# Optimization experiments

Hardware: AMD Instinct MI355X
Metric: run time of the kernel (lower is better)

## Reference

```python
import jax, jax.numpy as jnp
import numpy as np
from jax import lax

B, T_CAP, V, WD, H, L, IC = 256, 51, 10000, 512, 512, 2, 2048


def setup_inputs() -> dict:
    key = jax.random.key(0)
    ks = jax.random.split(key, 16)
    u01 = lambda k, s: jax.random.uniform(k, s, jnp.float32, -0.1, 0.1)
    sc = 1.0 / np.sqrt(H)
    uh = lambda k, s: jax.random.uniform(k, s, jnp.float32, -sc, sc)
    image_code = jax.random.normal(ks[0], (B, IC), jnp.float32)
    captions = jax.random.randint(ks[1], (B, T_CAP), 0, V)
    cap_lens = jax.random.randint(ks[2], (B,), 2, T_CAP + 1)
    cap_lens = cap_lens.at[0].set(T_CAP)  # guarantees max len == T_CAP (static scan length)
    return {
        "image_code": image_code,
        "captions": captions,
        "cap_lens": cap_lens,
        "embed_w": u01(ks[3], (V, WD)),
        "init_w": uh(ks[4], (L * H, IC)),
        "init_b": uh(ks[5], (L * H,)),
        "w_ih0": uh(ks[6], (3 * H, WD + IC)),
        "w_hh0": uh(ks[7], (3 * H, H)),
        "b_ih0": uh(ks[8], (3 * H,)),
        "b_hh0": uh(ks[9], (3 * H,)),
        "w_ih1": uh(ks[10], (3 * H, H)),
        "w_hh1": uh(ks[11], (3 * H, H)),
        "b_ih1": uh(ks[12], (3 * H,)),
        "b_hh1": uh(ks[13], (3 * H,)),
        "fc_w": u01(ks[14], (V, H)),
        "fc_b": jnp.zeros((V,), jnp.float32),
    }


def _gru_cell(x, h, w_ih, w_hh, b_ih, b_hh):
    # torch nn.GRU cell: gates ordered (r, z, n)
    gi = x @ w_ih.T + b_ih
    gh = h @ w_hh.T + b_hh
    i_r, i_z, i_n = jnp.split(gi, 3, axis=-1)
    h_r, h_z, h_n = jnp.split(gh, 3, axis=-1)
    r = jax.nn.sigmoid(i_r + h_r)
    z = jax.nn.sigmoid(i_z + h_z)
    n = jnp.tanh(i_n + r * h_n)
    return (1.0 - z) * n + z * h


def reference(image_code, captions, cap_lens, embed_w, init_w, init_b,
              w_ih0, w_hh0, b_ih0, b_hh0, w_ih1, w_hh1, b_ih1, b_hh1,
              fc_w, fc_b):
    b = image_code.shape[0]
    # sort by caption length, descending (ragged batch shrink in original)
    order = jnp.argsort(-cap_lens)
    sorted_lens = cap_lens[order]
    caps = captions[order]
    img = image_code[order]
    # init hidden: (L, B, H)
    h0 = (img @ init_w.T + init_b).reshape(b, L, H).transpose(1, 0, 2)
    lengths = sorted_lens - 1                      # decode steps per example
    T = captions.shape[1] - 1                      # static; equals lengths[0] by construction
    emb = embed_w[caps]                            # (B, T+1, WD)
    xs = jnp.swapaxes(emb[:, :T, :], 0, 1)         # (T, B, WD)
    mask_ts = jnp.arange(T)[:, None] < lengths[None, :]  # (T, B)
    params = [(w_ih0, w_hh0, b_ih0, b_hh0), (w_ih1, w_hh1, b_ih1, b_hh1)]

    def step(h, inp):
        x_emb, m = inp
        layer_in = jnp.concatenate([img, x_emb], axis=-1)  # (B, IC+WD)
        new_h = []
        for l, (wi, wh, bi, bh) in enumerate(params):
            hl = _gru_cell(layer_in, h[l], wi, wh, bi, bh)
            new_h.append(hl)
            layer_in = hl
        h_new = jnp.stack(new_h)
        # rows past their length keep their old hidden (equivalent to the
        # torch loop never touching rows beyond real_batch_size)
        h_new = jnp.where(m[None, :, None], h_new, h)
        preds = layer_in @ fc_w.T + fc_b           # dropout is identity in eval
        preds = jnp.where(m[:, None], preds, 0.0)  # predictions stay zero past length
        return h_new, preds

    _, preds = lax.scan(step, h0, (xs, mask_ts))   # preds: (T, B, V)
    predictions = jnp.swapaxes(preds, 0, 1)        # (B, T, V)
    return predictions, caps, lengths, order
```

## Files before the change

kernel.cpp:

```cpp
#include <hip/hip_runtime.h>
#include <hip/hip_bf16.h>

#define BB   256
#define TCAP 51
#define TT   50
#define VV   10000
#define WDIM 512
#define HH   512
#define ICC  2048
#define G3H  1536
#define FCP  8

typedef __attribute__((ext_vector_type(8))) short short8v;
typedef __attribute__((ext_vector_type(4))) float f32x4;

__device__ __forceinline__ unsigned short f2bf(float f) {
    unsigned u; __builtin_memcpy(&u, &f, 4);
    unsigned r = (u + 0x7FFFu + ((u >> 16) & 1u)) >> 16;
    return (unsigned short)r;
}
__device__ __forceinline__ float bf2f(unsigned short b) {
    unsigned u = ((unsigned)b) << 16; float f; __builtin_memcpy(&f, &u, 4); return f;
}
__device__ __forceinline__ short8v cvt8(float4 a, float4 b) {
    union { unsigned short u[8]; short8v v; } o;
    o.u[0] = f2bf(a.x); o.u[1] = f2bf(a.y); o.u[2] = f2bf(a.z); o.u[3] = f2bf(a.w);
    o.u[4] = f2bf(b.x); o.u[5] = f2bf(b.y); o.u[6] = f2bf(b.z); o.u[7] = f2bf(b.w);
    return o.v;
}
__device__ __forceinline__ float sigm(float x) { return 1.f / (1.f + expf(-x)); }

__global__ void sort_kernel(const int* __restrict__ cap_lens, const int* __restrict__ captions,
                            int* __restrict__ order_ws, int* __restrict__ len_ws,
                            int* __restrict__ caps_ws, float* __restrict__ out,
                            size_t predN) {
    __shared__ int s_order[BB];
    int i = threadIdx.x;
    int li = cap_lens[i];
    int rank = 0;
    for (int j = 0; j < BB; ++j) {
        int lj = cap_lens[j];
        rank += (lj > li) || (lj == li && j < i);
    }
    s_order[rank] = i;
    __syncthreads();
    int src = s_order[i];
    order_ws[i] = src;
    int len = cap_lens[src] - 1;
    len_ws[i] = len;
    for (int t = 0; t < TCAP; ++t) {
        int c = captions[src * TCAP + t];
        caps_ws[i * TCAP + t] = c;
        out[predN + (size_t)i * TCAP + t] = (float)c;
    }
    out[predN + (size_t)BB * TCAP + i]      = (float)len;
    out[predN + (size_t)BB * TCAP + BB + i] = (float)src;
}

__global__ void gather_imgb(const float* __restrict__ image_code, const int* __restrict__ order_ws,
                            unsigned short* __restrict__ imgb) {
    int i = blockIdx.x * 256 + threadIdx.x;
    int p = i >> 8, c8 = (i & 255) << 3;
    const float* s = image_code + (size_t)order_ws[p] * ICC + c8;
    float4 v0 = *(const float4*)s, v1 = *(const float4*)(s + 4);
    *(short8v*)&imgb[(size_t)p * ICC + c8] = cvt8(v0, v1);
}

__global__ void cvt_mat(const float* __restrict__ src, int src_ld, int src_off,
                        unsigned short* __restrict__ dst, int dst_ld, int dst_off,
                        int cols, int n8) {
    int i = blockIdx.x * 256 + threadIdx.x;
    if (i < n8) {
        int cpr = cols >> 3;
        int row = i / cpr, c8 = (i - row * cpr) << 3;
        const float* s = src + (size_t)row * src_ld + src_off + c8;
        float4 v0 = *(const float4*)s, v1 = *(const float4*)(s + 4);
        *(short8v*)&dst[(size_t)row * dst_ld + dst_off + c8] = cvt8(v0, v1);
    }
}

__global__ __launch_bounds__(256) void gemm_front(
    const unsigned short* __restrict__ imgb,
    const unsigned short* __restrict__ wcomb,
    const float* __restrict__ init_b,
    const float* __restrict__ b_ih0,
    unsigned short* __restrict__ h0s0,
    unsigned short* __restrict__ h1s0,
    float* __restrict__ gi_img) {
    const int p0 = blockIdx.y * 64;
    const int c0 = blockIdx.x * 64;
    const int tid = threadIdx.x;
    __shared__ unsigned short As[64][64 + FCP], Bs[64][64 + FCP];
    const int lane = tid & 63, w = tid >> 6;
    f32x4 acc[4] = {};
    for (int k0 = 0; k0 < ICC; k0 += 64) {
#pragma unroll
        for (int v = 0; v < 2; ++v) {
            int e = tid + v * 256;
            int rr = e >> 3, kk = (e & 7) * 8;
            *(short8v*)&As[rr][kk] = *(const short8v*)&imgb[(size_t)(p0 + rr) * ICC + k0 + kk];
            *(short8v*)&Bs[rr][kk] = *(const short8v*)&wcomb[(size_t)(c0 + rr) * ICC + k0 + kk];
        }
        __syncthreads();
#pragma unroll
        for (int ks = 0; ks < 64; ks += 32) {
            short8v a = *(const short8v*)&As[w * 16 + (lane & 15)][ks + (lane >> 4) * 8];
#pragma unroll
            for (int n = 0; n < 4; ++n) {
                short8v b = *(const short8v*)&Bs[n * 16 + (lane & 15)][ks + (lane >> 4) * 8];
                acc[n] = __builtin_amdgcn_mfma_f32_16x16x32_bf16(a, b, acc[n], 0, 0, 0);
            }
        }
        __syncthreads();
    }
#pragma unroll
    for (int n = 0; n < 4; ++n) {
        int cc = c0 + n * 16 + (lane & 15);
#pragma unroll
        for (int r = 0; r < 4; ++r) {
            int pr = p0 + w * 16 + (lane >> 4) * 4 + r;
            float v = acc[n][r];
            if (cc < 1024) {
                v += init_b[cc];
                unsigned short b = f2bf(v);
                if (cc < 512) h0s0[(size_t)pr * 512 + cc] = b;
                else          h1s0[(size_t)pr * 512 + (cc - 512)] = b;
            } else {
                gi_img[(size_t)pr * G3H + (cc - 1024)] = v + b_ih0[cc - 1024];
            }
        }
    }
}

__global__ __launch_bounds__(256) void gemm_giemb(
    const unsigned short* __restrict__ embb,
    const unsigned short* __restrict__ wihe,
    const float* __restrict__ gi_img,
    const int* __restrict__ caps_ws, const int* __restrict__ len_ws,
    float* __restrict__ gi_all) {
    const int r0 = blockIdx.y * 64;
    const int t = r0 >> 8, p0 = r0 & 255;
    if (len_ws[p0] <= t) return;
    const int c0 = blockIdx.x * 64;
    const int tid = threadIdx.x;
    __shared__ unsigned short As[64][64 + FCP], Bs[64][64 + FCP];
    __shared__ int s_arow[64];
    if (tid < 64) s_arow[tid] = caps_ws[(p0 + tid) * TCAP + t];
    __syncthreads();
    const int lane = tid & 63, w = tid >> 6;
    f32x4 acc[4] = {};
    for (int k0 = 0; k0 < WDIM; k0 += 64) {
#pragma unroll
        for (int v = 0; v < 2; ++v) {
            int e = tid + v * 256;
            int rr = e >> 3, kk = (e & 7) * 8;
            *(short8v*)&As[rr][kk] = *(const short8v*)&embb[(size_t)s_arow[rr] * WDIM + k0 + kk];
            *(short8v*)&Bs[rr][kk] = *(const short8v*)&wihe[(size_t)(c0 + rr) * WDIM + k0 + kk];
        }
        __syncthreads();
#pragma unroll
        for (int ks = 0; ks < 64; ks += 32) {
            short8v a = *(const short8v*)&As[w * 16 + (lane & 15)][ks + (lane >> 4) * 8];
#pragma unroll
            for (int n = 0; n < 4; ++n) {
                short8v b = *(const short8v*)&Bs[n * 16 + (lane & 15)][ks + (lane >> 4) * 8];
                acc[n] = __builtin_amdgcn_mfma_f32_16x16x32_bf16(a, b, acc[n], 0, 0, 0);
            }
        }
        __syncthreads();
    }
#pragma unroll
    for (int n = 0; n < 4; ++n) {
        int cc = c0 + n * 16 + (lane & 15);
#pragma unroll
        for (int r = 0; r < 4; ++r) {
            int pr = p0 + w * 16 + (lane >> 4) * 4 + r;
            if (t < len_ws[pr])
                gi_all[((size_t)t * BB + pr) * G3H + cc] = acc[n][r] + gi_img[(size_t)pr * G3H + cc];
        }
    }
}

__global__ __launch_bounds__(256, 1) void gru_fc_stage(int s,
    const unsigned short* __restrict__ h0_rd, unsigned short* __restrict__ h0_wr,
    float* __restrict__ gx_wr, const float* __restrict__ gx_rd,
    const unsigned short* __restrict__ h1_rd, unsigned short* __restrict__ h1_wr,
    unsigned short* __restrict__ h1x,
    const unsigned short* __restrict__ whh0b,
    const unsigned short* __restrict__ wih1b,
    const unsigned short* __restrict__ whh1b,
    const float* __restrict__ b_hh0, const float* __restrict__ gi_all,
    const float* __restrict__ b_ih1, const float* __restrict__ b_hh1,
    const unsigned short* __restrict__ fcwb,
    const float* __restrict__ fc_b,
    float* __restrict__ out,
    const int* __restrict__ len_ws) {
    __shared__ __align__(16) unsigned char smem_raw[55296];
    const int bid = blockIdx.x;
    const int tid = threadIdx.x, lane = tid & 63, w = tid >> 6;

    if (bid < 96) {
        const int role = bid >> 5;
        const int sub = bid & 31;
        const int cc0 = (sub & 7) * 64;
        const int p0 = (sub >> 3) * 64;
        const int t = s - role;
        if (t < 0 || t >= TT) return;
        if (len_ws[p0] <= t) return;
        unsigned short (*Bs)[3][64][72] =
            reinterpret_cast<unsigned short (*)[3][64][72]>(smem_raw);
        const unsigned short* Arows = (role == 2) ? h1_rd : h0_rd;
        const unsigned short* Bw = (role == 0) ? whh0b : (role == 1) ? wih1b : whh1b;
        const int rr0 = tid >> 3, kk0 = (tid & 7) * 8;

        const int arow = p0 + w * 16 + (lane & 15);
        const int akoff = (lane >> 4) * 8;
        short8v af[16];
#pragma unroll
        for (int kc = 0; kc < 8; ++kc) {
            af[kc * 2]     = *(const short8v*)&Arows[(size_t)arow * 512 + kc * 64 + akoff];
            af[kc * 2 + 1] = *(const short8v*)&Arows[(size_t)arow * 512 + kc * 64 + 32 + akoff];
        }

        f32x4 aG0[4] = {}, aG1[4] = {}, aG2[4] = {};
        short8v pb[2][6];

#define LOADB(SL, KC) {                                                              \
    size_t ko = (size_t)(KC) * 64 + kk0;                                             \
    pb[SL][0] = *(const short8v*)&Bw[(size_t)(cc0 + rr0) * 512 + ko];                \
    pb[SL][1] = *(const short8v*)&Bw[(size_t)(cc0 + rr0 + 32) * 512 + ko];           \
    pb[SL][2] = *(const short8v*)&Bw[(size_t)(512 + cc0 + rr0) * 512 + ko];          \
    pb[SL][3] = *(const short8v*)&Bw[(size_t)(512 + cc0 + rr0 + 32) * 512 + ko];     \
    pb[SL][4] = *(const short8v*)&Bw[(size_t)(1024 + cc0 + rr0) * 512 + ko];         \
    pb[SL][5] = *(const short8v*)&Bw[(size_t)(1024 + cc0 + rr0 + 32) * 512 + ko]; }

        LOADB(0, 0);
        LOADB(1, 1);
#pragma unroll
        for (int kc = 0; kc < 8; ++kc) {
            const int sl = kc & 1;
            *(short8v*)&Bs[sl][0][rr0][kk0]      = pb[sl][0];
            *(short8v*)&Bs[sl][0][rr0 + 32][kk0] = pb[sl][1];
            *(short8v*)&Bs[sl][1][rr0][kk0]      = pb[sl][2];
            *(short8v*)&Bs[sl][1][rr0 + 32][kk0] = pb[sl][3];
            *(short8v*)&Bs[sl][2][rr0][kk0]      = pb[sl][4];
            *(short8v*)&Bs[sl][2][rr0 + 32][kk0] = pb[sl][5];
            __syncthreads();
            if (kc < 6) LOADB(sl, kc + 2);
#pragma unroll
            for (int ks = 0; ks < 2; ++ks) {
                short8v a = af[kc * 2 + ks];
#pragma unroll
                for (int n = 0; n < 4; ++n) {
                    int br = n * 16 + (lane & 15), bk = ks * 32 + (lane >> 4) * 8;
                    short8v b0 = *(const short8v*)&Bs[sl][0][br][bk];
                    aG0[n] = __builtin_amdgcn_mfma_f32_16x16x32_bf16(a, b0, aG0[n], 0, 0, 0);
                    short8v b1 = *(const short8v*)&Bs[sl][1][br][bk];
                    aG1[n] = __builtin_amdgcn_mfma_f32_16x16x32_bf16(a, b1, aG1[n], 0, 0, 0);
                    short8v b2 = *(const short8v*)&Bs[sl][2][br][bk];
                    aG2[n] = __builtin_amdgcn_mfma_f32_16x16x32_bf16(a, b2, aG2[n], 0, 0, 0);
                }
            }
        }
#undef LOADB

        if (role == 0) {
#pragma unroll
            for (int n = 0; n < 4; ++n) {
                int cc = cc0 + n * 16 + (lane & 15);
                float bR = b_hh0[cc], bZ = b_hh0[512 + cc], bN = b_hh0[1024 + cc];
#pragma unroll
                for (int r = 0; r < 4; ++r) {
                    int p = p0 + w * 16 + (lane >> 4) * 4 + r;
                    const float* gi = gi_all + ((size_t)t * BB + p) * G3H;
                    float rr_ = sigm(gi[cc] + aG0[n][r] + bR);
                    float zz  = sigm(gi[512 + cc] + aG1[n][r] + bZ);
                    float nn  = tanhf(gi[1024 + cc] + rr_ * (aG2[n][r] + bN));
                    float hold = bf2f(h0_rd[(size_t)p * 512 + cc]);
                    float hnew = (t < len_ws[p]) ? (1.f - zz) * nn + zz * hold : hold;
                    h0_wr[(size_t)p * 512 + cc] = f2bf(hnew);
                }
            }
        } else if (role == 1) {
#pragma unroll
            for (int n = 0; n < 4; ++n) {
                int cc = cc0 + n * 16 + (lane & 15);
                float bR = b_ih1[cc], bZ = b_ih1[512 + cc], bN = b_ih1[1024 + cc];
#pragma unroll
                for (int r = 0; r < 4; ++r) {
                    int p = p0 + w * 16 + (lane >> 4) * 4 + r;
                    float* gx = gx_wr + (size_t)p * G3H;
                    gx[cc]        = aG0[n][r] + bR;
                    gx[512 + cc]  = aG1[n][r] + bZ;
                    gx[1024 + cc] = aG2[n][r] + bN;
                }
            }
        } else {
#pragma unroll
            for (int n = 0; n < 4; ++n) {
                int cc = cc0 + n * 16 + (lane & 15);
                float bR = b_hh1[cc], bZ = b_hh1[512 + cc], bN = b_hh1[1024 + cc];
#pragma unroll
                for (int r = 0; r < 4; ++r) {
                    int p = p0 + w * 16 + (lane >> 4) * 4 + r;
                    const float* gx = gx_rd + (size_t)p * G3H;
                    float rr_ = sigm(gx[cc] + aG0[n][r] + bR);
                    float zz  = sigm(gx[512 + cc] + aG1[n][r] + bZ);
                    float nn  = tanhf(gx[1024 + cc] + rr_ * (aG2[n][r] + bN));
                    float hold = bf2f(h1_rd[(size_t)p * 512 + cc]);
                    float hnew = (t < len_ws[p]) ? (1.f - zz) * nn + zz * hold : hold;
                    unsigned short hb = f2bf(hnew);
                    h1_wr[(size_t)p * 512 + cc] = hb;
                    h1x[((size_t)t * BB + p) * 512 + cc] = hb;
                }
            }
        }
        return;
    }

    const int t = s - 3;
    if (t < 0 || t >= TT) return;
    const int idx = bid - 96;
    const int c0 = (idx % 157) * 64;
    const int p0 = (idx / 157) * 128;
    if (len_ws[p0] <= t) {
        for (int e = tid; e < 128 * 16; e += 256) {
            int rl = e >> 4, c = c0 + (e & 15) * 4;
            if (c < VV) {
                float4 z = {0.f, 0.f, 0.f, 0.f};
                *(float4*)&out[((size_t)(p0 + rl) * TT + t) * VV + c] = z;
            }
        }
        return;
    }
    unsigned short (*As1)[64 + FCP] = reinterpret_cast<unsigned short (*)[64 + FCP]>(smem_raw);
    unsigned short (*As2)[64 + FCP] =
        reinterpret_cast<unsigned short (*)[64 + FCP]>(smem_raw + 9216);
    unsigned short (*Bsf)[64 + FCP] =
        reinterpret_cast<unsigned short (*)[64 + FCP]>(smem_raw + 18432);
    f32x4 acc1[4] = {}, acc2[4] = {};
    for (int k0 = 0; k0 < HH; k0 += 64) {
#pragma unroll
        for (int v = 0; v < 2; ++v) {
            int e = tid + v * 256;
            int rr = e >> 3, kk = (e & 7) * 8;
            *(short8v*)&As1[rr][kk] =
                *(const short8v*)&h1x[((size_t)(t * BB + p0 + rr)) * HH + k0 + kk];
            *(short8v*)&As2[rr][kk] =
                *(const short8v*)&h1x[((size_t)(t * BB + p0 + 64 + rr)) * HH + k0 + kk];
            int bc = c0 + rr;
            short8v bv = {};
            if (bc < VV) bv = *(const short8v*)&fcwb[(size_t)bc * HH + k0 + kk];
            *(short8v*)&Bsf[rr][kk] = bv;
        }
        __syncthreads();
#pragma unroll
        for (int ks = 0; ks < 64; ks += 32) {
            short8v a1 = *(const short8v*)&As1[w * 16 + (lane & 15)][ks + (lane >> 4) * 8];
            short8v a2 = *(const short8v*)&As2[w * 16 + (lane & 15)][ks + (lane >> 4) * 8];
#pragma unroll
            for (int n = 0; n < 4; ++n) {
                short8v b = *(const short8v*)&Bsf[n * 16 + (lane & 15)][ks + (lane >> 4) * 8];
                acc1[n] = __builtin_amdgcn_mfma_f32_16x16x32_bf16(a1, b, acc1[n], 0, 0, 0);
                acc2[n] = __builtin_amdgcn_mfma_f32_16x16x32_bf16(a2, b, acc2[n], 0, 0, 0);
            }
        }
        __syncthreads();
    }
#pragma unroll
    for (int n = 0; n < 4; ++n) {
        int c = c0 + n * 16 + (lane & 15);
        if (c < VV) {
            float bias = fc_b[c];
#pragma unroll
            for (int r = 0; r < 4; ++r) {
                int pr1 = p0 + w * 16 + (lane >> 4) * 4 + r;
                int pr2 = pr1 + 64;
                bool a1 = (t < len_ws[pr1]);
                bool a2 = (t < len_ws[pr2]);
                out[((size_t)pr1 * TT + t) * VV + c] = a1 ? (acc1[n][r] + bias) : 0.f;
                out[((size_t)pr2 * TT + t) * VV + c] = a2 ? (acc2[n][r] + bias) : 0.f;
            }
        }
    }
}

extern "C" void kernel_launch(void* const* d_in, const int* in_sizes, int n_in,
                              void* d_out, int out_size, void* d_ws, size_t ws_size,
                              hipStream_t stream) {
    const float* image_code = (const float*)d_in[0];
    const int*   captions   = (const int*)d_in[1];
    const int*   cap_lens   = (const int*)d_in[2];
    const float* embed_w    = (const float*)d_in[3];
    const float* init_w     = (const float*)d_in[4];
    const float* init_b     = (const float*)d_in[5];
    const float* w_ih0      = (const float*)d_in[6];
    const float* w_hh0      = (const float*)d_in[7];
    const float* b_ih0      = (const float*)d_in[8];
    const float* b_hh0      = (const float*)d_in[9];
    const float* w_ih1      = (const float*)d_in[10];
    const float* w_hh1      = (const float*)d_in[11];
    const float* b_ih1      = (const float*)d_in[12];
    const float* b_hh1      = (const float*)d_in[13];
    const float* fc_w       = (const float*)d_in[14];
    const float* fc_b       = (const float*)d_in[15];
    float* out = (float*)d_out;

    const size_t tail = (size_t)BB * TCAP + 2 * BB;
    const size_t predN = (size_t)out_size - tail;

    char* ws = (char*)d_ws;
    int*   order_ws = (int*)(ws + 0);
    int*   len_ws   = (int*)(ws + 1024);
    int*   caps_ws  = (int*)(ws + 2048);
    unsigned short* h0s[2] = {(unsigned short*)(ws + 54272),  (unsigned short*)(ws + 316416)};
    unsigned short* h1s[2] = {(unsigned short*)(ws + 578560), (unsigned short*)(ws + 840704)};
    float* gxb[2] = {(float*)(ws + 1102848), (float*)(ws + 2675712)};
    float* gi_img   = (float*)(ws + 4248576);
    float* gi_all   = (float*)(ws + 5821440);
    unsigned short* h1x  = (unsigned short*)(ws + 84464640);
    unsigned short* fcwb = (unsigned short*)(ws + 97571840);
    unsigned short* whh0b_s = (unsigned short*)(ws + 110000128);
    unsigned short* wih1b_s = (unsigned short*)(ws + 111572992);
    unsigned short* whh1b_s = (unsigned short*)(ws + 113145856);

    char* ob = (char*)d_out;
    unsigned short* imgb   = (unsigned short*)(ob + 0);
    unsigned short* wihe   = (unsigned short*)(ob + 1048576);
    unsigned short* wcomb  = (unsigned short*)(ob + 4194304);
    unsigned short* embb   = (unsigned short*)(ob + 16777216);

    dim3 blk(256);
    hipLaunchKernelGGL(sort_kernel, dim3(1), blk, 0, stream,
                       cap_lens, captions, order_ws, len_ws, caps_ws, out, predN);
    hipLaunchKernelGGL(gather_imgb, dim3(256), blk, 0, stream, image_code, order_ws, imgb);
    hipLaunchKernelGGL(cvt_mat, dim3(1024), blk, 0, stream,
                       init_w, ICC, 0, wcomb, ICC, 0, ICC, 1024 * ICC / 8);
    hipLaunchKernelGGL(cvt_mat, dim3(1536), blk, 0, stream,
                       w_ih0, ICC + WDIM, 0, wcomb + (size_t)1024 * ICC, ICC, 0, ICC, G3H * ICC / 8);
    hipLaunchKernelGGL(cvt_mat, dim3(384), blk, 0, stream,
                       w_ih0, ICC + WDIM, ICC, wihe, WDIM, 0, WDIM, G3H * WDIM / 8);
    hipLaunchKernelGGL(cvt_mat, dim3(2500), blk, 0, stream,
                       embed_w, WDIM, 0, embb, WDIM, 0, WDIM, VV * WDIM / 8);
    hipLaunchKernelGGL(cvt_mat, dim3(2500), blk, 0, stream,
                       fc_w, WDIM, 0, fcwb, WDIM, 0, WDIM, VV * WDIM / 8);
    hipLaunchKernelGGL(cvt_mat, dim3(384), blk, 0, stream,
                       w_hh0, WDIM, 0, whh0b_s, WDIM, 0, WDIM, G3H * WDIM / 8);
    hipLaunchKernelGGL(cvt_mat, dim3(384), blk, 0, stream,
                       w_ih1, WDIM, 0, wih1b_s, WDIM, 0, WDIM, G3H * WDIM / 8);
    hipLaunchKernelGGL(cvt_mat, dim3(384), blk, 0, stream,
                       w_hh1, WDIM, 0, whh1b_s, WDIM, 0, WDIM, G3H * WDIM / 8);

    hipLaunchKernelGGL(gemm_front, dim3(40, 4), blk, 0, stream,
                       imgb, wcomb, init_b, b_ih0, h0s[0], h1s[0], gi_img);
    hipLaunchKernelGGL(gemm_giemb, dim3(24, 200), blk, 0, stream,
                       embb, wihe, gi_img, caps_ws, len_ws, gi_all);

    for (int s = 0; s <= TT + 2; ++s) {
        int q = s & 1;
        hipLaunchKernelGGL(gru_fc_stage, dim3(96 + 314), blk, 0, stream, s,
                           h0s[q], h0s[q ^ 1],
                           gxb[q ^ 1], gxb[q],
                           h1s[q], h1s[q ^ 1],
                           h1x, whh0b_s, wih1b_s, whh1b_s,
                           b_hh0, gi_all, b_ih1, b_hh1,
                           fcwb, fc_b, out, len_ws);
    }
}
```

Baseline: 1.125 ms.

## Double-buffer LDS tiles with register prefetch in the FC projection loop

Restructures the FC projection K-loop so global loads of the h1 and fc_w tiles for chunk k+2 are issued into registers while the MFMAs run on chunk k. Two LDS slots alternate, which removes the trailing barrier per iteration and fully unrolls the 8 chunks. This is meant to hide global-load latency behind the matrix math. The cost is higher register pressure from the 12 prefetched vectors and roughly double the shared-memory footprint, which could reduce occupancy or exceed the existing shared allocation.

New measurement: 1.141 ms. About the same (+1.4%).

```diff
diff --git a/kernel.cpp b/kernel.cpp
--- a/kernel.cpp
+++ b/kernel.cpp
@@ -333,40 +333,53 @@
         }
         return;
     }
-    unsigned short (*As1)[64 + FCP] = reinterpret_cast<unsigned short (*)[64 + FCP]>(smem_raw);
-    unsigned short (*As2)[64 + FCP] =
-        reinterpret_cast<unsigned short (*)[64 + FCP]>(smem_raw + 9216);
-    unsigned short (*Bsf)[64 + FCP] =
-        reinterpret_cast<unsigned short (*)[64 + FCP]>(smem_raw + 18432);
+    unsigned short* smu = reinterpret_cast<unsigned short*>(smem_raw);
+    const int rr0 = tid >> 3, kk0 = (tid & 7) * 8;
     f32x4 acc1[4] = {}, acc2[4] = {};
-    for (int k0 = 0; k0 < HH; k0 += 64) {
-#pragma unroll
-        for (int v = 0; v < 2; ++v) {
-            int e = tid + v * 256;
-            int rr = e >> 3, kk = (e & 7) * 8;
-            *(short8v*)&As1[rr][kk] =
-                *(const short8v*)&h1x[((size_t)(t * BB + p0 + rr)) * HH + k0 + kk];
-            *(short8v*)&As2[rr][kk] =
-                *(const short8v*)&h1x[((size_t)(t * BB + p0 + 64 + rr)) * HH + k0 + kk];
-            int bc = c0 + rr;
-            short8v bv = {};
-            if (bc < VV) bv = *(const short8v*)&fcwb[(size_t)bc * HH + k0 + kk];
-            *(short8v*)&Bsf[rr][kk] = bv;
-        }
+    short8v pf[2][6];
+
+#define LOADF(SL, KC) {                                                                   \
+    size_t ko = (size_t)(KC) * 64 + kk0;                                                  \
+    pf[SL][0] = *(const short8v*)&h1x[((size_t)(t * BB + p0 + rr0)) * 512 + ko];          \
+    pf[SL][1] = *(const short8v*)&h1x[((size_t)(t * BB + p0 + rr0 + 32)) * 512 + ko];     \
+    pf[SL][2] = *(const short8v*)&h1x[((size_t)(t * BB + p0 + 64 + rr0)) * 512 + ko];     \
+    pf[SL][3] = *(const short8v*)&h1x[((size_t)(t * BB + p0 + 64 + rr0 + 32)) * 512 + ko];\
+    int bc1 = c0 + rr0, bc2 = c0 + rr0 + 32;                                              \
+    short8v bv1 = {}, bv2 = {};                                                           \
+    if (bc1 < VV) bv1 = *(const short8v*)&fcwb[(size_t)bc1 * 512 + ko];                   \
+    if (bc2 < VV) bv2 = *(const short8v*)&fcwb[(size_t)bc2 * 512 + ko];                   \
+    pf[SL][4] = bv1; pf[SL][5] = bv2; }
+
+    LOADF(0, 0);
+    LOADF(1, 1);
+#pragma unroll
+    for (int kc = 0; kc < 8; ++kc) {
+        const int sl = kc & 1;
+        unsigned short* tA1 = smu + (sl * 3 + 0) * 4608;
+        unsigned short* tA2 = smu + (sl * 3 + 1) * 4608;
+        unsigned short* tB  = smu + (sl * 3 + 2) * 4608;
+        *(short8v*)&tA1[rr0 * 72 + kk0]        = pf[sl][0];
+        *(short8v*)&tA1[(rr0 + 32) * 72 + kk0] = pf[sl][1];
+        *(short8v*)&tA2[rr0 * 72 + kk0]        = pf[sl][2];
+        *(short8v*)&tA2[(rr0 + 32) * 72 + kk0] = pf[sl][3];
+        *(short8v*)&tB[rr0 * 72 + kk0]         = pf[sl][4];
+        *(short8v*)&tB[(rr0 + 32) * 72 + kk0]  = pf[sl][5];
         __syncthreads();
-#pragma unroll
-        for (int ks = 0; ks < 64; ks += 32) {
-            short8v a1 = *(const short8v*)&As1[w * 16 + (lane & 15)][ks + (lane >> 4) * 8];
-            short8v a2 = *(const short8v*)&As2[w * 16 + (lane & 15)][ks + (lane >> 4) * 8];
-#pragma unroll
-            for (int n = 0; n < 4; ++n) {
-                short8v b = *(const short8v*)&Bsf[n * 16 + (lane & 15)][ks + (lane >> 4) * 8];
+        if (kc < 6) LOADF(sl, kc + 2);
+#pragma unroll
+        for (int ks = 0; ks < 2; ++ks) {
+            int ar = w * 16 + (lane & 15), ak = ks * 32 + (lane >> 4) * 8;
+            short8v a1 = *(const short8v*)&tA1[ar * 72 + ak];
+            short8v a2 = *(const short8v*)&tA2[ar * 72 + ak];
+#pragma unroll
+            for (int n = 0; n < 4; ++n) {
+                short8v b = *(const short8v*)&tB[(n * 16 + (lane & 15)) * 72 + ak];
                 acc1[n] = __builtin_amdgcn_mfma_f32_16x16x32_bf16(a1, b, acc1[n], 0, 0, 0);
                 acc2[n] = __builtin_amdgcn_mfma_f32_16x16x32_bf16(a2, b, acc2[n], 0, 0, 0);
             }
         }
-        __syncthreads();
-    }
+    }
+#undef LOADF
 #pragma unroll
     for (int n = 0; n < 4; ++n) {
         int c = c0 + n * 16 + (lane & 15);
```
